# Optimization experiments

Measured on AMD Instinct MI355X. Metric: run time of the kernel, lower is better.

Reference implementation:

```python
import jax
import jax.numpy as jnp
from jax import lax
import numpy as np

INPUT_SIZE = 2
COND_SIZE = 4
HIDDEN = 128
LATENT = 32
DEC_IN = INPUT_SIZE + LATENT + COND_SIZE + 1  # 39
DT = 0.05


def setup_inputs() -> dict:
    key = jax.random.key(0)
    ks = jax.random.split(key, 9)
    B = 8192
    s = 1.0 / np.sqrt(HIDDEN)  # PyTorch LSTM init scale
    z = jax.random.normal(ks[0], (B, LATENT), jnp.float32)
    condition = jax.random.normal(ks[1], (B, COND_SIZE), jnp.float32)
    start_point = jax.random.normal(ks[2], (B, INPUT_SIZE), jnp.float32)
    W_ih = jax.random.uniform(ks[3], (4 * HIDDEN, DEC_IN), jnp.float32, -s, s)
    W_hh = jax.random.uniform(ks[4], (4 * HIDDEN, HIDDEN), jnp.float32, -s, s)
    b_ih = jax.random.uniform(ks[5], (4 * HIDDEN,), jnp.float32, -s, s)
    b_hh = jax.random.uniform(ks[6], (4 * HIDDEN,), jnp.float32, -s, s)
    W_out = jax.random.uniform(ks[7], (INPUT_SIZE, HIDDEN), jnp.float32, -s, s)
    b_out = jax.random.uniform(ks[8], (INPUT_SIZE,), jnp.float32, -s, s)
    return {
        "z": z, "condition": condition, "start_point": start_point,
        "W_ih": W_ih, "W_hh": W_hh, "b_ih": b_ih, "b_hh": b_hh,
        "W_out": W_out, "b_out": b_out, "seq_len": 2048,
    }


def reference(z, condition, start_point, W_ih, W_hh, b_ih, b_hh, W_out, b_out, seq_len):
    B = z.shape[0]
    dt = jnp.full((B, 1), DT, dtype=z.dtype)  # constant delta_t per step
    # precompute the static part of the per-step input projection: [z, cond, dt]
    # columns of W_ih: [x(2) | z(32) | cond(4) | dt(1)]
    static_in = jnp.concatenate([z, condition, dt], axis=-1)  # [B, 37]
    static_proj = static_in @ W_ih[:, INPUT_SIZE:].T + b_ih + b_hh  # [B, 4H]
    W_ih_x = W_ih[:, :INPUT_SIZE]  # [4H, 2]

    def step(carry, _):
        x_t, h, c = carry
        gates = x_t @ W_ih_x.T + static_proj + h @ W_hh.T  # [B, 4H]
        i, f, g, o = jnp.split(gates, 4, axis=-1)
        i = jax.nn.sigmoid(i)
        f = jax.nn.sigmoid(f)
        g = jnp.tanh(g)
        o = jax.nn.sigmoid(o)
        c = f * c + i * g
        h = o * jnp.tanh(c)
        x_next = h @ W_out.T + b_out  # [B, input_size]
        return (x_next, h, c), x_next

    h0 = jnp.zeros((B, HIDDEN), z.dtype)
    c0 = jnp.zeros((B, HIDDEN), z.dtype)
    _, ys = lax.scan(step, (start_point, h0, c0), None, length=seq_len)
    return jnp.transpose(ys, (1, 0, 2))  # [B, seq_len, input_size]
```

## Files before the change

### kernel.cpp

```cpp
#include <hip/hip_runtime.h>

typedef short bf16x8 __attribute__((ext_vector_type(8)));
typedef float f32x4 __attribute__((ext_vector_type(4)));

#define LOG2E 1.44269504088896340736f

__device__ __forceinline__ unsigned short f2bf(float x) {
    unsigned u = __builtin_bit_cast(unsigned, x);
    return (unsigned short)((u + 0x7fffu + ((u >> 16) & 1u)) >> 16);
}

__global__ __launch_bounds__(512, 2)
void lstm_persist(const float* __restrict__ zP, const float* __restrict__ condP,
                  const float* __restrict__ startP, const float* __restrict__ WihP,
                  const float* __restrict__ WhhP, const float* __restrict__ bihP,
                  const float* __restrict__ bhhP, const float* __restrict__ WoutP,
                  const float* __restrict__ boutP, float* __restrict__ outP)
{
    __shared__ unsigned short hist[8 * 32 * 128];
    char* const lds = (char*)hist;

    const int tid  = threadIdx.x;
    const int wave = tid >> 6;
    const int lane = tid & 63;
    const int lo   = lane & 15;
    const int gq   = lane >> 4;
    const int r0   = blockIdx.x * 32;
    const int hid0 = wave * 16;

    float wx0[4], wx1[4], bias[4];
    bf16x8 bfrag[4][4];
    #pragma unroll
    for (int s = 0; s < 4; ++s) {
        const int col = s * 128 + hid0 + lo;
        wx0[s]  = WihP[col * 39 + 0];
        wx1[s]  = WihP[col * 39 + 1];
        bias[s] = bihP[col] + bhhP[col];
        #pragma unroll
        for (int kt = 0; kt < 4; ++kt) {
            bf16x8 f;
            #pragma unroll
            for (int j = 0; j < 8; ++j) {
                const int k = kt * 32 + gq * 8 + j;
                const float w = WhhP[col * 128 + k]
                              + wx0[s] * WoutP[k] + wx1[s] * WoutP[128 + k];
                f[j] = (short)f2bf(w);
            }
            bfrag[s][kt] = f;
        }
    }

    bf16x8 wof[4];
    #pragma unroll
    for (int kt = 0; kt < 4; ++kt) {
        bf16x8 f;
        #pragma unroll
        for (int j = 0; j < 8; ++j) {
            const int k = kt * 32 + gq * 8 + j;
            f[j] = (lo < 2) ? (short)f2bf(WoutP[lo * 128 + k]) : (short)0;
        }
        wof[kt] = f;
    }
    const float bo = (lo < 2) ? boutP[lo] : 0.0f;

    f32x4 sp[2][4];
    #pragma unroll
    for (int m = 0; m < 2; ++m)
        #pragma unroll
        for (int s = 0; s < 4; ++s)
            #pragma unroll
            for (int rr = 0; rr < 4; ++rr)
                sp[m][s][rr] = bias[s];

    for (int j = 0; j < 32; ++j) {
        float w[4];
        #pragma unroll
        for (int s = 0; s < 4; ++s) w[s] = WihP[(s * 128 + hid0 + lo) * 39 + 2 + j];
        #pragma unroll
        for (int m = 0; m < 2; ++m)
            #pragma unroll
            for (int rr = 0; rr < 4; ++rr) {
                const int row = r0 + m * 16 + gq * 4 + rr;
                const float si = zP[row * 32 + j];
                #pragma unroll
                for (int s = 0; s < 4; ++s) sp[m][s][rr] += si * w[s];
            }
    }
    for (int j = 0; j < 4; ++j) {
        float w[4];
        #pragma unroll
        for (int s = 0; s < 4; ++s) w[s] = WihP[(s * 128 + hid0 + lo) * 39 + 34 + j];
        #pragma unroll
        for (int m = 0; m < 2; ++m)
            #pragma unroll
            for (int rr = 0; rr < 4; ++rr) {
                const int row = r0 + m * 16 + gq * 4 + rr;
                const float si = condP[row * 4 + j];
                #pragma unroll
                for (int s = 0; s < 4; ++s) sp[m][s][rr] += si * w[s];
            }
    }
    {
        #pragma unroll
        for (int s = 0; s < 4; ++s) {
            const float w = 0.05f * WihP[(s * 128 + hid0 + lo) * 39 + 38];
            #pragma unroll
            for (int m = 0; m < 2; ++m)
                #pragma unroll
                for (int rr = 0; rr < 4; ++rr) sp[m][s][rr] += w;
        }
    }

    int wroff[2][4];
    #pragma unroll
    for (int m = 0; m < 2; ++m)
        #pragma unroll
        for (int rr = 0; rr < 4; ++rr) {
            const int row = m * 16 + gq * 4 + rr;
            wroff[m][rr] = (row * 256 + (hid0 + lo) * 2) ^ ((row & 7) << 4);
        }
    int rdoff[4];
    #pragma unroll
    for (int kt = 0; kt < 4; ++kt)
        rdoff[kt] = (lo * 256 + kt * 64 + gq * 16) ^ ((lo & 7) << 4);
    int xrdoff[4];
    #pragma unroll
    for (int kt = 0; kt < 4; ++kt)
        xrdoff[kt] = ((wave * 32 + lo) * 256 + kt * 64 + gq * 16) ^ ((lo & 7) << 4);

    f32x4 cst[2];
    cst[0] = f32x4{0.f, 0.f, 0.f, 0.f};
    cst[1] = f32x4{0.f, 0.f, 0.f, 0.f};

    auto tail = [&](f32x4 (&acc)[2][4], const int wbase) {
        #pragma unroll
        for (int m = 0; m < 2; ++m) {
            float h[4];
            #pragma unroll
            for (int rr = 0; rr < 4; ++rr) {
                const float ig = acc[m][0][rr], fg = acc[m][1][rr];
                const float gg = acc[m][2][rr], og = acc[m][3][rr];
                const float si = __builtin_amdgcn_rcpf(1.0f + __builtin_amdgcn_exp2f(ig * -LOG2E));
                const float sf = __builtin_amdgcn_rcpf(1.0f + __builtin_amdgcn_exp2f(fg * -LOG2E));
                const float so = __builtin_amdgcn_rcpf(1.0f + __builtin_amdgcn_exp2f(og * -LOG2E));
                const float tg = 1.0f - 2.0f * __builtin_amdgcn_rcpf(1.0f + __builtin_amdgcn_exp2f(gg * (2.0f * LOG2E)));
                const float cn = sf * cst[m][rr] + si * tg;
                cst[m][rr] = cn;
                const float tc = 1.0f - 2.0f * __builtin_amdgcn_rcpf(1.0f + __builtin_amdgcn_exp2f(cn * (2.0f * LOG2E)));
                h[rr] = so * tc;
            }
            unsigned p01, p23;
            asm("v_cvt_pk_bf16_f32 %0, %1, %2" : "=v"(p01) : "v"(h[0]), "v"(h[1]));
            asm("v_cvt_pk_bf16_f32 %0, %1, %2" : "=v"(p23) : "v"(h[2]), "v"(h[3]));
            *(unsigned short*)(lds + wbase + wroff[m][0]) = (unsigned short)(p01 & 0xffffu);
            *(unsigned short*)(lds + wbase + wroff[m][1]) = (unsigned short)(p01 >> 16);
            *(unsigned short*)(lds + wbase + wroff[m][2]) = (unsigned short)(p23 & 0xffffu);
            *(unsigned short*)(lds + wbase + wroff[m][3]) = (unsigned short)(p23 >> 16);
        }
    };

    {
        f32x4 acc0[2][4];
        #pragma unroll
        for (int m = 0; m < 2; ++m)
            #pragma unroll
            for (int s = 0; s < 4; ++s) acc0[m][s] = sp[m][s];
        #pragma unroll
        for (int m = 0; m < 2; ++m)
            #pragma unroll
            for (int rr = 0; rr < 4; ++rr) {
                const int row = r0 + m * 16 + gq * 4 + rr;
                const float x0 = startP[row * 2 + 0];
                const float x1 = startP[row * 2 + 1];
                #pragma unroll
                for (int s = 0; s < 4; ++s)
                    acc0[m][s][rr] += x0 * wx0[s] + x1 * wx1[s];
            }
        tail(acc0, 0);
    }
    #pragma unroll
    for (int s = 0; s < 4; ++s) {
        const float bx = wx0[s] * boutP[0] + wx1[s] * boutP[1];
        #pragma unroll
        for (int m = 0; m < 2; ++m)
            #pragma unroll
            for (int rr = 0; rr < 4; ++rr) sp[m][s][rr] += bx;
    }
    __syncthreads();

    #pragma unroll 1
    for (int t = 1; t < 2048; ++t) {
        const int rbase = ((t - 1) & 7) * 8192;
        const int wbase = (t & 7) * 8192;

        bf16x8 af[2][4];
        #pragma unroll
        for (int kt = 0; kt < 4; ++kt) {
            af[0][kt] = __builtin_bit_cast(bf16x8, *(const f32x4*)(lds + rbase + rdoff[kt]));
            af[1][kt] = __builtin_bit_cast(bf16x8, *(const f32x4*)(lds + rbase + rdoff[kt] + 4096));
        }
        f32x4 acc[2][4];
        #pragma unroll
        for (int m = 0; m < 2; ++m)
            #pragma unroll
            for (int s = 0; s < 4; ++s) {
                f32x4 a = sp[m][s];
                #pragma unroll
                for (int kt = 0; kt < 4; ++kt)
                    a = __builtin_amdgcn_mfma_f32_16x16x32_bf16(af[m][kt], bfrag[s][kt], a, 0, 0, 0);
                acc[m][s] = a;
            }
        tail(acc, wbase);
        __syncthreads();

        if ((t & 7) == 7) {
            f32x4 xacc[2];
            xacc[0] = f32x4{0.f, 0.f, 0.f, 0.f};
            xacc[1] = f32x4{0.f, 0.f, 0.f, 0.f};
            #pragma unroll
            for (int mt = 0; mt < 2; ++mt)
                #pragma unroll
                for (int kt = 0; kt < 4; ++kt) {
                    const bf16x8 a = __builtin_bit_cast(bf16x8,
                        *(const f32x4*)(lds + xrdoff[kt] + mt * 4096));
                    xacc[mt] = __builtin_amdgcn_mfma_f32_16x16x32_bf16(a, wof[kt], xacc[mt], 0, 0, 0);
                }
            const int tg = t - 7 + wave;
            if (lo < 2) {
                #pragma unroll
                for (int mt = 0; mt < 2; ++mt)
                    #pragma unroll
                    for (int rr = 0; rr < 4; ++rr) {
                        const int row = mt * 16 + gq * 4 + rr;
                        outP[(size_t)(r0 + row) * 4096 + tg * 2 + lo] = xacc[mt][rr] + bo;
                    }
            }
            __syncthreads();
        }
    }
}

extern "C" void kernel_launch(void* const* d_in, const int* in_sizes, int n_in,
                              void* d_out, int out_size, void* d_ws, size_t ws_size,
                              hipStream_t stream) {
    const float* z    = (const float*)d_in[0];
    const float* cond = (const float*)d_in[1];
    const float* strt = (const float*)d_in[2];
    const float* Wih  = (const float*)d_in[3];
    const float* Whh  = (const float*)d_in[4];
    const float* bih  = (const float*)d_in[5];
    const float* bhh  = (const float*)d_in[6];
    const float* Wout = (const float*)d_in[7];
    const float* bout = (const float*)d_in[8];
    float* out = (float*)d_out;

    hipLaunchKernelGGL(lstm_persist, dim3(256), dim3(512), 0, stream,
                       z, cond, strt, Wih, Whh, bih, bhh, Wout, bout, out);
}
```

Measured before the change: 3.190 ms.

## Halve rows per block to 16, doubling grid and fold gate scales into weights

Each block now handles 16 batch rows instead of 32, so the grid doubles to 512 blocks and launch bounds request 4 blocks per CU. The LDS history buffer halves, and the per-step work per wave drops to one M-tile of MFMAs. Separately, the sigmoid/tanh exponent scale factors (-log2e, 2log2e) are prescaled into the recurrent weights, input weights and static projection, removing multiplies from the serial tail. The intent is to shorten the per-step critical path and spread the recurrence over more CUs, at the cost of more blocks competing per CU and register pressure limits under the higher occupancy bound.

```diff
diff --git a/kernel.cpp b/kernel.cpp
--- a/kernel.cpp
+++ b/kernel.cpp
@@ -10,14 +10,14 @@
     return (unsigned short)((u + 0x7fffu + ((u >> 16) & 1u)) >> 16);
 }
 
-__global__ __launch_bounds__(512, 2)
+__global__ __launch_bounds__(512, 4)
 void lstm_persist(const float* __restrict__ zP, const float* __restrict__ condP,
                   const float* __restrict__ startP, const float* __restrict__ WihP,
                   const float* __restrict__ WhhP, const float* __restrict__ bihP,
                   const float* __restrict__ bhhP, const float* __restrict__ WoutP,
                   const float* __restrict__ boutP, float* __restrict__ outP)
 {
-    __shared__ unsigned short hist[8 * 32 * 128];
+    __shared__ unsigned short hist[8 * 16 * 128];
     char* const lds = (char*)hist;
 
     const int tid  = threadIdx.x;
@@ -25,16 +25,21 @@
     const int lane = tid & 63;
     const int lo   = lane & 15;
     const int gq   = lane >> 4;
-    const int r0   = blockIdx.x * 32;
+    const int r0   = blockIdx.x * 16;
     const int hid0 = wave * 16;
 
-    float wx0[4], wx1[4], bias[4];
+    const float K2 = 2.0f * LOG2E;
+    const float ss[4] = { -LOG2E, -LOG2E, 2.0f * LOG2E, -LOG2E };
+
+    float wxs0[4], wxs1[4], bias[4];
     bf16x8 bfrag[4][4];
     #pragma unroll
     for (int s = 0; s < 4; ++s) {
         const int col = s * 128 + hid0 + lo;
-        wx0[s]  = WihP[col * 39 + 0];
-        wx1[s]  = WihP[col * 39 + 1];
+        const float wx0 = WihP[col * 39 + 0];
+        const float wx1 = WihP[col * 39 + 1];
+        wxs0[s] = ss[s] * wx0;
+        wxs1[s] = ss[s] * wx1;
         bias[s] = bihP[col] + bhhP[col];
         #pragma unroll
         for (int kt = 0; kt < 4; ++kt) {
@@ -43,8 +48,8 @@
             for (int j = 0; j < 8; ++j) {
                 const int k = kt * 32 + gq * 8 + j;
                 const float w = WhhP[col * 128 + k]
-                              + wx0[s] * WoutP[k] + wx1[s] * WoutP[128 + k];
-                f[j] = (short)f2bf(w);
+                              + wx0 * WoutP[k] + wx1 * WoutP[128 + k];
+                f[j] = (short)f2bf(ss[s] * w);
             }
             bfrag[s][kt] = f;
         }
@@ -63,177 +68,141 @@
     }
     const float bo = (lo < 2) ? boutP[lo] : 0.0f;
 
-    f32x4 sp[2][4];
-    #pragma unroll
-    for (int m = 0; m < 2; ++m)
-        #pragma unroll
-        for (int s = 0; s < 4; ++s)
-            #pragma unroll
-            for (int rr = 0; rr < 4; ++rr)
-                sp[m][s][rr] = bias[s];
+    f32x4 sp[4];
+    #pragma unroll
+    for (int s = 0; s < 4; ++s)
+        #pragma unroll
+        for (int rr = 0; rr < 4; ++rr)
+            sp[s][rr] = bias[s];
 
     for (int j = 0; j < 32; ++j) {
         float w[4];
         #pragma unroll
         for (int s = 0; s < 4; ++s) w[s] = WihP[(s * 128 + hid0 + lo) * 39 + 2 + j];
         #pragma unroll
-        for (int m = 0; m < 2; ++m)
-            #pragma unroll
-            for (int rr = 0; rr < 4; ++rr) {
-                const int row = r0 + m * 16 + gq * 4 + rr;
-                const float si = zP[row * 32 + j];
-                #pragma unroll
-                for (int s = 0; s < 4; ++s) sp[m][s][rr] += si * w[s];
-            }
+        for (int rr = 0; rr < 4; ++rr) {
+            const int row = r0 + gq * 4 + rr;
+            const float si = zP[row * 32 + j];
+            #pragma unroll
+            for (int s = 0; s < 4; ++s) sp[s][rr] += si * w[s];
+        }
     }
     for (int j = 0; j < 4; ++j) {
         float w[4];
         #pragma unroll
         for (int s = 0; s < 4; ++s) w[s] = WihP[(s * 128 + hid0 + lo) * 39 + 34 + j];
         #pragma unroll
-        for (int m = 0; m < 2; ++m)
-            #pragma unroll
-            for (int rr = 0; rr < 4; ++rr) {
-                const int row = r0 + m * 16 + gq * 4 + rr;
-                const float si = condP[row * 4 + j];
-                #pragma unroll
-                for (int s = 0; s < 4; ++s) sp[m][s][rr] += si * w[s];
-            }
-    }
-    {
-        #pragma unroll
-        for (int s = 0; s < 4; ++s) {
-            const float w = 0.05f * WihP[(s * 128 + hid0 + lo) * 39 + 38];
-            #pragma unroll
-            for (int m = 0; m < 2; ++m)
-                #pragma unroll
-                for (int rr = 0; rr < 4; ++rr) sp[m][s][rr] += w;
-        }
-    }
-
-    int wroff[2][4];
-    #pragma unroll
-    for (int m = 0; m < 2; ++m)
-        #pragma unroll
-        for (int rr = 0; rr < 4; ++rr) {
-            const int row = m * 16 + gq * 4 + rr;
-            wroff[m][rr] = (row * 256 + (hid0 + lo) * 2) ^ ((row & 7) << 4);
-        }
+        for (int rr = 0; rr < 4; ++rr) {
+            const int row = r0 + gq * 4 + rr;
+            const float si = condP[row * 4 + j];
+            #pragma unroll
+            for (int s = 0; s < 4; ++s) sp[s][rr] += si * w[s];
+        }
+    }
+    #pragma unroll
+    for (int s = 0; s < 4; ++s) {
+        const float w = 0.05f * WihP[(s * 128 + hid0 + lo) * 39 + 38];
+        #pragma unroll
+        for (int rr = 0; rr < 4; ++rr) sp[s][rr] = ss[s] * (sp[s][rr] + w);
+    }
+
+    int wroff[4];
+    #pragma unroll
+    for (int rr = 0; rr < 4; ++rr) {
+        const int row = gq * 4 + rr;
+        wroff[rr] = (row * 256 + (hid0 + lo) * 2) ^ ((row & 7) << 4);
+    }
     int rdoff[4];
     #pragma unroll
     for (int kt = 0; kt < 4; ++kt)
         rdoff[kt] = (lo * 256 + kt * 64 + gq * 16) ^ ((lo & 7) << 4);
-    int xrdoff[4];
-    #pragma unroll
-    for (int kt = 0; kt < 4; ++kt)
-        xrdoff[kt] = ((wave * 32 + lo) * 256 + kt * 64 + gq * 16) ^ ((lo & 7) << 4);
-
-    f32x4 cst[2];
-    cst[0] = f32x4{0.f, 0.f, 0.f, 0.f};
-    cst[1] = f32x4{0.f, 0.f, 0.f, 0.f};
-
-    auto tail = [&](f32x4 (&acc)[2][4], const int wbase) {
-        #pragma unroll
-        for (int m = 0; m < 2; ++m) {
-            float h[4];
-            #pragma unroll
-            for (int rr = 0; rr < 4; ++rr) {
-                const float ig = acc[m][0][rr], fg = acc[m][1][rr];
-                const float gg = acc[m][2][rr], og = acc[m][3][rr];
-                const float si = __builtin_amdgcn_rcpf(1.0f + __builtin_amdgcn_exp2f(ig * -LOG2E));
-                const float sf = __builtin_amdgcn_rcpf(1.0f + __builtin_amdgcn_exp2f(fg * -LOG2E));
-                const float so = __builtin_amdgcn_rcpf(1.0f + __builtin_amdgcn_exp2f(og * -LOG2E));
-                const float tg = 1.0f - 2.0f * __builtin_amdgcn_rcpf(1.0f + __builtin_amdgcn_exp2f(gg * (2.0f * LOG2E)));
-                const float cn = sf * cst[m][rr] + si * tg;
-                cst[m][rr] = cn;
-                const float tc = 1.0f - 2.0f * __builtin_amdgcn_rcpf(1.0f + __builtin_amdgcn_exp2f(cn * (2.0f * LOG2E)));
-                h[rr] = so * tc;
-            }
-            unsigned p01, p23;
-            asm("v_cvt_pk_bf16_f32 %0, %1, %2" : "=v"(p01) : "v"(h[0]), "v"(h[1]));
-            asm("v_cvt_pk_bf16_f32 %0, %1, %2" : "=v"(p23) : "v"(h[2]), "v"(h[3]));
-            *(unsigned short*)(lds + wbase + wroff[m][0]) = (unsigned short)(p01 & 0xffffu);
-            *(unsigned short*)(lds + wbase + wroff[m][1]) = (unsigned short)(p01 >> 16);
-            *(unsigned short*)(lds + wbase + wroff[m][2]) = (unsigned short)(p23 & 0xffffu);
-            *(unsigned short*)(lds + wbase + wroff[m][3]) = (unsigned short)(p23 >> 16);
-        }
+
+    f32x4 cst = f32x4{0.f, 0.f, 0.f, 0.f};
+
+    auto tail = [&](f32x4 (&acc)[4], const int wbase) {
+        float h[4];
+        #pragma unroll
+        for (int rr = 0; rr < 4; ++rr) {
+            const float si = __builtin_amdgcn_rcpf(1.0f + __builtin_amdgcn_exp2f(acc[0][rr]));
+            const float sf = __builtin_amdgcn_rcpf(1.0f + __builtin_amdgcn_exp2f(acc[1][rr]));
+            const float rg = __builtin_amdgcn_rcpf(1.0f + __builtin_amdgcn_exp2f(acc[2][rr]));
+            const float so = __builtin_amdgcn_rcpf(1.0f + __builtin_amdgcn_exp2f(acc[3][rr]));
+            const float tg = __builtin_fmaf(rg, -2.0f, 1.0f);
+            const float cn = __builtin_fmaf(sf, cst[rr], si * tg);
+            cst[rr] = cn;
+            const float rc = __builtin_amdgcn_rcpf(1.0f + __builtin_amdgcn_exp2f(cn * K2));
+            const float tc = __builtin_fmaf(rc, -2.0f, 1.0f);
+            h[rr] = so * tc;
+        }
+        unsigned p01, p23;
+        asm("v_cvt_pk_bf16_f32 %0, %1, %2" : "=v"(p01) : "v"(h[0]), "v"(h[1]));
+        asm("v_cvt_pk_bf16_f32 %0, %1, %2" : "=v"(p23) : "v"(h[2]), "v"(h[3]));
+        *(unsigned short*)(lds + wbase + wroff[0]) = (unsigned short)(p01 & 0xffffu);
+        *(unsigned short*)(lds + wbase + wroff[1]) = (unsigned short)(p01 >> 16);
+        *(unsigned short*)(lds + wbase + wroff[2]) = (unsigned short)(p23 & 0xffffu);
+        *(unsigned short*)(lds + wbase + wroff[3]) = (unsigned short)(p23 >> 16);
     };
 
     {
-        f32x4 acc0[2][4];
-        #pragma unroll
-        for (int m = 0; m < 2; ++m)
-            #pragma unroll
-            for (int s = 0; s < 4; ++s) acc0[m][s] = sp[m][s];
-        #pragma unroll
-        for (int m = 0; m < 2; ++m)
-            #pragma unroll
-            for (int rr = 0; rr < 4; ++rr) {
-                const int row = r0 + m * 16 + gq * 4 + rr;
-                const float x0 = startP[row * 2 + 0];
-                const float x1 = startP[row * 2 + 1];
-                #pragma unroll
-                for (int s = 0; s < 4; ++s)
-                    acc0[m][s][rr] += x0 * wx0[s] + x1 * wx1[s];
-            }
+        f32x4 acc0[4];
+        #pragma unroll
+        for (int s = 0; s < 4; ++s) acc0[s] = sp[s];
+        #pragma unroll
+        for (int rr = 0; rr < 4; ++rr) {
+            const int row = r0 + gq * 4 + rr;
+            const float x0 = startP[row * 2 + 0];
+            const float x1 = startP[row * 2 + 1];
+            #pragma unroll
+            for (int s = 0; s < 4; ++s)
+                acc0[s][rr] += x0 * wxs0[s] + x1 * wxs1[s];
+        }
         tail(acc0, 0);
     }
     #pragma unroll
     for (int s = 0; s < 4; ++s) {
-        const float bx = wx0[s] * boutP[0] + wx1[s] * boutP[1];
-        #pragma unroll
-        for (int m = 0; m < 2; ++m)
-            #pragma unroll
-            for (int rr = 0; rr < 4; ++rr) sp[m][s][rr] += bx;
+        const float bx = wxs0[s] * boutP[0] + wxs1[s] * boutP[1];
+        #pragma unroll
+        for (int rr = 0; rr < 4; ++rr) sp[s][rr] += bx;
     }
     __syncthreads();
 
     #pragma unroll 1
     for (int t = 1; t < 2048; ++t) {
-        const int rbase = ((t - 1) & 7) * 8192;
-        const int wbase = (t & 7) * 8192;
-
-        bf16x8 af[2][4];
-        #pragma unroll
-        for (int kt = 0; kt < 4; ++kt) {
-            af[0][kt] = __builtin_bit_cast(bf16x8, *(const f32x4*)(lds + rbase + rdoff[kt]));
-            af[1][kt] = __builtin_bit_cast(bf16x8, *(const f32x4*)(lds + rbase + rdoff[kt] + 4096));
-        }
-        f32x4 acc[2][4];
-        #pragma unroll
-        for (int m = 0; m < 2; ++m)
-            #pragma unroll
-            for (int s = 0; s < 4; ++s) {
-                f32x4 a = sp[m][s];
-                #pragma unroll
-                for (int kt = 0; kt < 4; ++kt)
-                    a = __builtin_amdgcn_mfma_f32_16x16x32_bf16(af[m][kt], bfrag[s][kt], a, 0, 0, 0);
-                acc[m][s] = a;
-            }
+        const int rbase = ((t - 1) & 7) * 4096;
+        const int wbase = (t & 7) * 4096;
+
+        bf16x8 af[4];
+        #pragma unroll
+        for (int kt = 0; kt < 4; ++kt)
+            af[kt] = __builtin_bit_cast(bf16x8, *(const f32x4*)(lds + rbase + rdoff[kt]));
+
+        f32x4 acc[4];
+        #pragma unroll
+        for (int s = 0; s < 4; ++s) {
+            f32x4 a = sp[s];
+            #pragma unroll
+            for (int kt = 0; kt < 4; ++kt)
+                a = __builtin_amdgcn_mfma_f32_16x16x32_bf16(af[kt], bfrag[s][kt], a, 0, 0, 0);
+            acc[s] = a;
+        }
         tail(acc, wbase);
         __syncthreads();
 
         if ((t & 7) == 7) {
-            f32x4 xacc[2];
-            xacc[0] = f32x4{0.f, 0.f, 0.f, 0.f};
-            xacc[1] = f32x4{0.f, 0.f, 0.f, 0.f};
-            #pragma unroll
-            for (int mt = 0; mt < 2; ++mt)
-                #pragma unroll
-                for (int kt = 0; kt < 4; ++kt) {
-                    const bf16x8 a = __builtin_bit_cast(bf16x8,
-                        *(const f32x4*)(lds + xrdoff[kt] + mt * 4096));
-                    xacc[mt] = __builtin_amdgcn_mfma_f32_16x16x32_bf16(a, wof[kt], xacc[mt], 0, 0, 0);
-                }
+            f32x4 xacc = f32x4{0.f, 0.f, 0.f, 0.f};
+            #pragma unroll
+            for (int kt = 0; kt < 4; ++kt) {
+                const bf16x8 a = __builtin_bit_cast(bf16x8,
+                    *(const f32x4*)(lds + wave * 4096 + rdoff[kt]));
+                xacc = __builtin_amdgcn_mfma_f32_16x16x32_bf16(a, wof[kt], xacc, 0, 0, 0);
+            }
             const int tg = t - 7 + wave;
             if (lo < 2) {
                 #pragma unroll
-                for (int mt = 0; mt < 2; ++mt)
-                    #pragma unroll
-                    for (int rr = 0; rr < 4; ++rr) {
-                        const int row = mt * 16 + gq * 4 + rr;
-                        outP[(size_t)(r0 + row) * 4096 + tg * 2 + lo] = xacc[mt][rr] + bo;
-                    }
+                for (int rr = 0; rr < 4; ++rr) {
+                    const int row = gq * 4 + rr;
+                    outP[(size_t)(r0 + row) * 4096 + tg * 2 + lo] = xacc[rr] + bo;
+                }
             }
             __syncthreads();
         }
@@ -254,6 +223,6 @@
     const float* bout = (const float*)d_in[8];
     float* out = (float*)d_out;
 
-    hipLaunchKernelGGL(lstm_persist, dim3(256), dim3(512), 0, stream,
+    hipLaunchKernelGGL(lstm_persist, dim3(512), dim3(512), 0, stream,
                        z, cond, strt, Wih, Whh, bih, bhh, Wout, bout, out);
 }
```

Result: no change. 3.130 ms (-1.9%).
